# Performance work log

Measured on AMD Instinct MI355X. Metric: run time of the kernel, lower is better.

Reference implementation:

```python
import jax, jax.numpy as jnp
import numpy as np

N, M, D = 65536, 2048, 256

def setup_inputs() -> dict:
    key = jax.random.key(0)
    k1, k2 = jax.random.split(key)
    memory = jax.random.normal(k1, (M, D), dtype=jnp.float32)
    query = jax.random.normal(k2, (N, D), dtype=jnp.float32)
    return {"memory": memory, "query": query}

def reference(memory, query):
    # score: [N, M] = query @ memory^T
    score = jnp.matmul(query.astype(jnp.float32), memory.astype(jnp.float32).T)
    # softmax over memory slots (dim=1); scores are detached in the original
    softmax_score_memory = jax.nn.softmax(score, axis=1)
    # read from memory: [N, M] @ [M, D] -> [N, D]
    concat_memory = jnp.matmul(softmax_score_memory, memory)
    return concat_memory
```

## Files before the change

### kernel.cpp

```cpp
#include <hip/hip_runtime.h>

typedef _Float16 f16;
typedef __attribute__((ext_vector_type(8))) _Float16 f16x8;
typedef __attribute__((ext_vector_type(16))) float f32x16;
typedef __attribute__((ext_vector_type(4))) unsigned u32x4;

#define MM 2048
#define DD 256
#define LOG2E 1.44269504088896340736f

__device__ __forceinline__ void gload_lds16(const void* g, void* l) {
    __builtin_amdgcn_global_load_lds(
        (const __attribute__((address_space(1))) unsigned int*)g,
        (__attribute__((address_space(3))) unsigned int*)l, 16, 0, 0);
}
__device__ __forceinline__ f32x16 mfma32(f16x8 a, f16x8 b, f32x16 c) {
    return __builtin_amdgcn_mfma_f32_32x32x16_f16(a, b, c, 0, 0, 0);
}
__device__ __forceinline__ void plswap(unsigned& a, unsigned& b) {
    asm volatile("v_permlane32_swap_b32 %0, %1" : "+v"(a), "+v"(b));
}
__device__ __forceinline__ unsigned pk2(float a, float b) {
    return __builtin_bit_cast(unsigned, __builtin_amdgcn_cvt_pkrtz(a, b));
}

__global__ void prep_kernel(const float* __restrict__ mem,
                            f16* __restrict__ kprep, f16* __restrict__ vtprep) {
    int t = blockIdx.x * blockDim.x + threadIdx.x;
    if (t < 65536) {
        int b = t >> 10, r = t & 1023, u = r >> 5, kk = r & 31;
        const float* src = mem + (b * 32 + kk) * DD + u * 8;
        f16 o8[8];
#pragma unroll
        for (int e = 0; e < 8; ++e) o8[e] = (f16)src[e];
        *(f16x8*)(kprep + (size_t)t * 8) = *(f16x8*)o8;
    } else {
        int t2 = t - 65536;
        int b = t2 >> 10, r = t2 & 1023, u = r >> 8, d = r & 255;
        f16 o8[8];
#pragma unroll
        for (int e = 0; e < 8; ++e) o8[e] = (f16)mem[(b * 32 + u * 8 + e) * DD + d];
        *(f16x8*)(vtprep + (size_t)t2 * 8) = *(f16x8*)o8;
    }
}

__launch_bounds__(256, 2)
__global__ void attn_kernel(const float* __restrict__ q,
                            const f16* __restrict__ kprep,
                            const f16* __restrict__ vtprep,
                            float* __restrict__ out) {
    __shared__ __align__(16) f16 klds[2][8192];
    __shared__ __align__(16) f16 vtlds[2][8192];

    const int tid = threadIdx.x;
    const int w = __builtin_amdgcn_readfirstlane(tid >> 6);
    const int lane = tid & 63;
    const int h = lane >> 5;
    const int l31 = lane & 31;
    const int q0 = blockIdx.x * 128 + w * 32;

    f16x8 qf[16];
#pragma unroll
    for (int s = 0; s < 16; ++s) {
        const float* src = q + (size_t)(q0 + l31) * DD + s * 16 + h * 8;
        float4 a = *(const float4*)src;
        float4 b2 = *(const float4*)(src + 4);
        f16 t8[8] = {(f16)a.x, (f16)a.y, (f16)a.z, (f16)a.w,
                     (f16)b2.x, (f16)b2.y, (f16)b2.z, (f16)b2.w};
        qf[s] = *(f16x8*)t8;
    }

    f32x16 o[8];
#pragma unroll
    for (int dt = 0; dt < 8; ++dt) o[dt] = (f32x16)(0.f);
    float lpart = 0.f, mrun = -1e30f;
    f16x8 pa0 = (f16x8)(f16)0.f, pa1 = (f16x8)(f16)0.f;

#define STAGE_K(b_, c_)                                                   \
    do {                                                                  \
        const f16* s_ = kprep + (size_t)(b_)*8192;                        \
        _Pragma("unroll")                                                 \
        for (int i_ = 0; i_ < 4; ++i_)                                    \
            gload_lds16(s_ + i_ * 2048 + w * 512 + lane * 8,              \
                        &klds[c_][i_ * 2048 + w * 512]);                  \
    } while (0)
#define STAGE_VT(b_, c_)                                                  \
    do {                                                                  \
        const f16* s_ = vtprep + (size_t)(b_)*8192;                       \
        _Pragma("unroll")                                                 \
        for (int i_ = 0; i_ < 4; ++i_)                                    \
            gload_lds16(s_ + i_ * 2048 + w * 512 + lane * 8,              \
                        &vtlds[c_][i_ * 2048 + w * 512]);                 \
    } while (0)

#define SOFTMAX_PACK(s_)                                                       \
    do {                                                                       \
        float sm_ = s_[0];                                                     \
        _Pragma("unroll") for (int r_ = 1; r_ < 16; ++r_)                      \
            sm_ = fmaxf(sm_, s_[r_]);                                          \
        sm_ *= LOG2E;                                                          \
        if (__any(sm_ > mrun + 8.0f)) {                                        \
            sm_ = fmaxf(sm_, __shfl_xor(sm_, 32));                             \
            const float mn_ = fmaxf(mrun, sm_);                                \
            const float fct_ = __builtin_amdgcn_exp2f(mrun - mn_);             \
            mrun = mn_;                                                        \
            lpart *= fct_;                                                     \
            float fr_[16];                                                     \
            _Pragma("unroll") for (int r_ = 0; r_ < 16; ++r_)                  \
                fr_[r_] = __shfl(fct_, (r_ & 3) + 8 * (r_ >> 2) + 4 * h, 32);  \
            _Pragma("unroll") for (int dt_ = 0; dt_ < 8; ++dt_)                \
                _Pragma("unroll") for (int r_ = 0; r_ < 16; ++r_)              \
                    o[dt_][r_] *= fr_[r_];                                     \
        }                                                                      \
        float p_[16], rs_ = 0.f;                                               \
        _Pragma("unroll") for (int r_ = 0; r_ < 16; ++r_) {                    \
            p_[r_] = __builtin_amdgcn_exp2f(                                   \
                __builtin_fmaf(s_[r_], LOG2E, -mrun));                         \
            rs_ += p_[r_];                                                     \
        }                                                                      \
        lpart += rs_;                                                          \
        unsigned c0_ = pk2(p_[0], p_[1]), c1_ = pk2(p_[2], p_[3]);             \
        unsigned c2_ = pk2(p_[4], p_[5]), c3_ = pk2(p_[6], p_[7]);             \
        unsigned c4_ = pk2(p_[8], p_[9]), c5_ = pk2(p_[10], p_[11]);           \
        unsigned c6_ = pk2(p_[12], p_[13]), c7_ = pk2(p_[14], p_[15]);         \
        plswap(c0_, c2_); plswap(c1_, c3_);                                    \
        plswap(c4_, c6_); plswap(c5_, c7_);                                    \
        u32x4 k0_ = {c0_, c1_, c2_, c3_}, k1_ = {c4_, c5_, c6_, c7_};          \
        pa0 = __builtin_bit_cast(f16x8, k0_);                                  \
        pa1 = __builtin_bit_cast(f16x8, k1_);                                  \
    } while (0)

#define RD_K(st_) (*(const f16x8*)(&klds[c][((2 * (st_) + h) * 32 + l31) * 8]))
#define RD_V0(g_) (*(const f16x8*)(&vtlds[c ^ 1][((0 + h) * 256 + (g_)*32 + l31) * 8]))
#define RD_V1(g_) (*(const f16x8*)(&vtlds[c ^ 1][((2 + h) * 256 + (g_)*32 + l31) * 8]))

    STAGE_K(0, 0);

    {
        const int c = 0;
        __syncthreads();
        STAGE_K(1, 1);
        STAGE_VT(0, 0);
        f32x16 s = (f32x16)(0.f);
        __builtin_amdgcn_s_setprio(1);
#pragma unroll
        for (int st = 0; st < 16; ++st) s = mfma32(RD_K(st), qf[st], s);
        __builtin_amdgcn_s_setprio(0);
        SOFTMAX_PACK(s);
    }

    for (int b = 1; b < 64; ++b) {
        const int c = b & 1;
        __syncthreads();
        if (b < 63) STAGE_K(b + 1, c ^ 1);
        STAGE_VT(b, c);

        f32x16 s = (f32x16)(0.f);
        __builtin_amdgcn_s_setprio(1);
        f16x8 v0c = RD_V0(0), v1c = RD_V1(0);
#pragma unroll
        for (int g = 0; g < 8; ++g) {
            f16x8 v0n, v1n;
            if (g < 7) { v0n = RD_V0(g + 1); v1n = RD_V1(g + 1); }
            s = mfma32(RD_K(2 * g), qf[2 * g], s);
            o[g] = mfma32(pa0, v0c, o[g]);
            s = mfma32(RD_K(2 * g + 1), qf[2 * g + 1], s);
            o[g] = mfma32(pa1, v1c, o[g]);
            if (g < 7) { v0c = v0n; v1c = v1n; }
        }
        __builtin_amdgcn_s_setprio(0);
        SOFTMAX_PACK(s);
    }

    __syncthreads();
    __builtin_amdgcn_s_setprio(1);
    {
        const int c = 0;
#pragma unroll
        for (int g = 0; g < 8; ++g) {
            o[g] = mfma32(pa0, RD_V0(g), o[g]);
            o[g] = mfma32(pa1, RD_V1(g), o[g]);
        }
    }
    __builtin_amdgcn_s_setprio(0);

    const float ltot = lpart + __shfl_xor(lpart, 32);
    const float inv = 1.0f / ltot;
    float invr[16];
#pragma unroll
    for (int r = 0; r < 16; ++r)
        invr[r] = __shfl(inv, (r & 3) + 8 * (r >> 2) + 4 * h, 32);
#pragma unroll
    for (int dt = 0; dt < 8; ++dt)
#pragma unroll
        for (int r = 0; r < 16; ++r) {
            const int qrow = (r & 3) + 8 * (r >> 2) + 4 * h;
            out[(size_t)(q0 + qrow) * DD + dt * 32 + l31] = o[dt][r] * invr[r];
        }
}

extern "C" void kernel_launch(void* const* d_in, const int* in_sizes, int n_in,
                              void* d_out, int out_size, void* d_ws, size_t ws_size,
                              hipStream_t stream) {
    const float* memory = (const float*)d_in[0];
    const float* query = (const float*)d_in[1];
    float* out = (float*)d_out;
    f16* kprep = (f16*)d_ws;
    f16* vtprep = kprep + (size_t)MM * DD;
    prep_kernel<<<512, 256, 0, stream>>>(memory, kprep, vtprep);
    attn_kernel<<<512, 256, 0, stream>>>(query, kprep, vtprep, out);
}
```

Measured before the change: 157.9 us.

## Use 8-wave blocks with quad-buffered K/V staging, two tiles per barrier

```diff
diff --git a/kernel.cpp b/kernel.cpp
--- a/kernel.cpp
+++ b/kernel.cpp
@@ -44,20 +44,20 @@
     }
 }
 
-__launch_bounds__(256, 2)
+__launch_bounds__(512, 2)
 __global__ void attn_kernel(const float* __restrict__ q,
                             const f16* __restrict__ kprep,
                             const f16* __restrict__ vtprep,
                             float* __restrict__ out) {
-    __shared__ __align__(16) f16 klds[2][8192];
-    __shared__ __align__(16) f16 vtlds[2][8192];
+    __shared__ __align__(16) f16 klds[4][8192];
+    __shared__ __align__(16) f16 vtlds[4][8192];
 
     const int tid = threadIdx.x;
     const int w = __builtin_amdgcn_readfirstlane(tid >> 6);
     const int lane = tid & 63;
     const int h = lane >> 5;
     const int l31 = lane & 31;
-    const int q0 = blockIdx.x * 128 + w * 32;
+    const int q0 = blockIdx.x * 256 + w * 32;
 
     f16x8 qf[16];
 #pragma unroll
@@ -76,21 +76,43 @@
     float lpart = 0.f, mrun = -1e30f;
     f16x8 pa0 = (f16x8)(f16)0.f, pa1 = (f16x8)(f16)0.f;
 
-#define STAGE_K(b_, c_)                                                   \
+#define STAGE_K(t_)                                                       \
     do {                                                                  \
-        const f16* s_ = kprep + (size_t)(b_)*8192;                        \
+        const f16* s_ = kprep + (size_t)(t_)*8192;                        \
         _Pragma("unroll")                                                 \
-        for (int i_ = 0; i_ < 4; ++i_)                                    \
-            gload_lds16(s_ + i_ * 2048 + w * 512 + lane * 8,              \
-                        &klds[c_][i_ * 2048 + w * 512]);                  \
-    } while (0)
-#define STAGE_VT(b_, c_)                                                  \
+        for (int i_ = 0; i_ < 2; ++i_)                                    \
+            gload_lds16(s_ + i_ * 4096 + w * 512 + lane * 8,              \
+                        &klds[(t_) & 3][i_ * 4096 + w * 512]);            \
+    } while (0)
+#define STAGE_VT(t_)                                                      \
     do {                                                                  \
-        const f16* s_ = vtprep + (size_t)(b_)*8192;                       \
+        const f16* s_ = vtprep + (size_t)(t_)*8192;                       \
         _Pragma("unroll")                                                 \
-        for (int i_ = 0; i_ < 4; ++i_)                                    \
-            gload_lds16(s_ + i_ * 2048 + w * 512 + lane * 8,              \
-                        &vtlds[c_][i_ * 2048 + w * 512]);                 \
+        for (int i_ = 0; i_ < 2; ++i_)                                    \
+            gload_lds16(s_ + i_ * 4096 + w * 512 + lane * 8,              \
+                        &vtlds[(t_) & 3][i_ * 4096 + w * 512]);           \
+    } while (0)
+
+#define QK(t_, s_)                                                            \
+    do {                                                                      \
+        const f16* kb_ = &klds[(t_) & 3][0];                                  \
+        _Pragma("unroll")                                                     \
+        for (int st_ = 0; st_ < 16; ++st_) {                                  \
+            f16x8 ak_ = *(const f16x8*)(kb_ + ((2 * st_ + h) * 32 + l31) * 8);\
+            s_ = mfma32(ak_, qf[st_], s_);                                    \
+        }                                                                     \
+    } while (0)
+
+#define PV(t_)                                                                 \
+    do {                                                                       \
+        const f16* vb_ = &vtlds[(t_) & 3][0];                                  \
+        _Pragma("unroll")                                                      \
+        for (int dt_ = 0; dt_ < 8; ++dt_) {                                    \
+            f16x8 v0_ = *(const f16x8*)(vb_ + ((0 + h) * 256 + dt_ * 32 + l31) * 8); \
+            f16x8 v1_ = *(const f16x8*)(vb_ + ((2 + h) * 256 + dt_ * 32 + l31) * 8); \
+            o[dt_] = mfma32(pa0, v0_, o[dt_]);                                 \
+            o[dt_] = mfma32(pa1, v1_, o[dt_]);                                 \
+        }                                                                      \
     } while (0)
 
 #define SOFTMAX_PACK(s_)                                                       \
@@ -130,58 +152,35 @@
         pa1 = __builtin_bit_cast(f16x8, k1_);                                  \
     } while (0)
 
-#define RD_K(st_) (*(const f16x8*)(&klds[c][((2 * (st_) + h) * 32 + l31) * 8]))
-#define RD_V0(g_) (*(const f16x8*)(&vtlds[c ^ 1][((0 + h) * 256 + (g_)*32 + l31) * 8]))
-#define RD_V1(g_) (*(const f16x8*)(&vtlds[c ^ 1][((2 + h) * 256 + (g_)*32 + l31) * 8]))
-
-    STAGE_K(0, 0);
-
-    {
-        const int c = 0;
+    STAGE_K(0);
+    STAGE_K(1);
+    STAGE_VT(0);
+
+    for (int p = 0; p < 32; ++p) {
+        const int t0 = 2 * p, t1 = 2 * p + 1;
         __syncthreads();
-        STAGE_K(1, 1);
-        STAGE_VT(0, 0);
-        f32x16 s = (f32x16)(0.f);
+        if (p < 31) { STAGE_K(t0 + 2); STAGE_K(t1 + 2); }
+        STAGE_VT(t1);
+        if (p < 31) STAGE_VT(t1 + 1);
+
         __builtin_amdgcn_s_setprio(1);
-#pragma unroll
-        for (int st = 0; st < 16; ++st) s = mfma32(RD_K(st), qf[st], s);
+        f32x16 s0 = (f32x16)(0.f);
+        QK(t0, s0);
+        if (p) PV(t0 - 1);
         __builtin_amdgcn_s_setprio(0);
-        SOFTMAX_PACK(s);
-    }
-
-    for (int b = 1; b < 64; ++b) {
-        const int c = b & 1;
-        __syncthreads();
-        if (b < 63) STAGE_K(b + 1, c ^ 1);
-        STAGE_VT(b, c);
-
-        f32x16 s = (f32x16)(0.f);
+        SOFTMAX_PACK(s0);
+
         __builtin_amdgcn_s_setprio(1);
-        f16x8 v0c = RD_V0(0), v1c = RD_V1(0);
-#pragma unroll
-        for (int g = 0; g < 8; ++g) {
-            f16x8 v0n, v1n;
-            if (g < 7) { v0n = RD_V0(g + 1); v1n = RD_V1(g + 1); }
-            s = mfma32(RD_K(2 * g), qf[2 * g], s);
-            o[g] = mfma32(pa0, v0c, o[g]);
-            s = mfma32(RD_K(2 * g + 1), qf[2 * g + 1], s);
-            o[g] = mfma32(pa1, v1c, o[g]);
-            if (g < 7) { v0c = v0n; v1c = v1n; }
-        }
+        f32x16 s1 = (f32x16)(0.f);
+        QK(t1, s1);
+        PV(t0);
         __builtin_amdgcn_s_setprio(0);
-        SOFTMAX_PACK(s);
+        SOFTMAX_PACK(s1);
     }
 
     __syncthreads();
     __builtin_amdgcn_s_setprio(1);
-    {
-        const int c = 0;
-#pragma unroll
-        for (int g = 0; g < 8; ++g) {
-            o[g] = mfma32(pa0, RD_V0(g), o[g]);
-            o[g] = mfma32(pa1, RD_V1(g), o[g]);
-        }
-    }
+    PV(63);
     __builtin_amdgcn_s_setprio(0);
 
     const float ltot = lpart + __shfl_xor(lpart, 32);
@@ -208,5 +207,5 @@
     f16* kprep = (f16*)d_ws;
     f16* vtprep = kprep + (size_t)MM * DD;
     prep_kernel<<<512, 256, 0, stream>>>(memory, kprep, vtprep);
-    attn_kernel<<<512, 256, 0, stream>>>(query, kprep, vtprep, out);
-}
+    attn_kernel<<<256, 512, 0, stream>>>(query, kprep, vtprep, out);
+}
```

After: 150.9 us. 1.05x faster.
